# Kernel tuning notes

Hardware: AMD Instinct MI355X
Metric: run time of the kernel (lower is better)

Reference implementation:

```python
import jax, jax.numpy as jnp
import numpy as np

N_NODES = 50000
N_EDGES = 1600000
IN_FEATS = 128
H_FEATS = 128


def setup_inputs() -> dict:
    key = jax.random.key(0)
    ks = jax.random.split(key, 10)
    feat = jax.random.normal(ks[0], (N_NODES, IN_FEATS), dtype=jnp.float32)
    src = jax.random.randint(ks[1], (N_EDGES,), 0, N_NODES, dtype=jnp.int32)
    dst = jax.random.randint(ks[2], (N_EDGES,), 0, N_NODES, dtype=jnp.int32)
    s1 = 1.0 / np.sqrt(IN_FEATS)
    s2 = 1.0 / np.sqrt(H_FEATS)
    W_self1 = jax.random.uniform(ks[3], (IN_FEATS, H_FEATS), jnp.float32, -s1, s1)
    W_neigh1 = jax.random.uniform(ks[4], (IN_FEATS, H_FEATS), jnp.float32, -s1, s1)
    b1 = jnp.zeros((H_FEATS,), jnp.float32)
    W_self2 = jax.random.uniform(ks[5], (H_FEATS, H_FEATS), jnp.float32, -s2, s2)
    W_neigh2 = jax.random.uniform(ks[6], (H_FEATS, H_FEATS), jnp.float32, -s2, s2)
    b2 = jnp.zeros((H_FEATS,), jnp.float32)
    W_fc = jax.random.uniform(ks[7], (H_FEATS, IN_FEATS), jnp.float32, -s2, s2)
    b_fc = jax.random.uniform(ks[8], (IN_FEATS,), jnp.float32, -s2, s2)
    return {
        "feat": feat, "src": src, "dst": dst,
        "W_self1": W_self1, "W_neigh1": W_neigh1, "b1": b1,
        "W_self2": W_self2, "W_neigh2": W_neigh2, "b2": b2,
        "W_fc": W_fc, "b_fc": b_fc,
    }


def _mean_agg(h, src, dst):
    # segment-mean of src features onto dst nodes; zero-in-degree -> 0 (deg clamped to 1)
    msg = jnp.take(h, src, axis=0)                      # [E, d] gather (irregular)
    summ = jax.ops.segment_sum(msg, dst, num_segments=N_NODES)  # [N, d]
    deg = jax.ops.segment_sum(jnp.ones((src.shape[0],), h.dtype), dst, num_segments=N_NODES)
    return summ / jnp.maximum(deg, 1.0)[:, None]


def _sage(h, src, dst, W_self, W_neigh, b):
    h_neigh = _mean_agg(h, src, dst)
    return h @ W_self + h_neigh @ W_neigh + b


def reference(feat, src, dst, W_self1, W_neigh1, b1, W_self2, W_neigh2, b2, W_fc, b_fc):
    h = _sage(feat, src, dst, W_self1, W_neigh1, b1)
    h = jax.nn.relu(h)
    h = _sage(h, src, dst, W_self2, W_neigh2, b2)
    return h @ W_fc + b_fc
```

## Files before the change

kernel.cpp:

```cpp
#include <hip/hip_runtime.h>
#include <hip/hip_bf16.h>

#define NN 50000
#define NPAD 50008
#define NE 1600000
#define F 128
#define CAP 96
#define NBUCK 391
#define BCAP 5120
#define PADIDX 0xC350C350u

typedef short short8 __attribute__((ext_vector_type(8)));
typedef float f32x4 __attribute__((ext_vector_type(4)));
typedef float f32x2 __attribute__((ext_vector_type(2)));
typedef unsigned short u16x4 __attribute__((ext_vector_type(4)));
typedef unsigned short u16x8 __attribute__((ext_vector_type(8)));

__device__ inline unsigned short bf16rne(float f) {
  unsigned u = __builtin_bit_cast(unsigned, f);
  u += 0x7FFFu + ((u >> 16) & 1u);
  return (unsigned short)(u >> 16);
}
__device__ inline float bf16f(unsigned short s) {
  unsigned u = ((unsigned)s) << 16;
  return __builtin_bit_cast(float, u);
}
__device__ inline float bflo(unsigned v) { return __builtin_bit_cast(float, v << 16); }
__device__ inline float bfhi(unsigned v) { return __builtin_bit_cast(float, v & 0xFFFF0000u); }

__global__ void zero_misc(int* __restrict__ gcur, unsigned short* __restrict__ hbf) {
  int i = threadIdx.x;
  if (i < NBUCK) gcur[i] = 0;
  int p = i >> 7, r = NN + ((i >> 4) & 7), d = i & 15;
  ((unsigned*)hbf)[((size_t)p * NPAD + r) * 16 + d] = 0u;
}

__global__ void compose_all(const float* __restrict__ Ws2, const float* __restrict__ Wn2,
                            const float* __restrict__ b2, const float* __restrict__ Wfc,
                            const float* __restrict__ bfc,
                            float* __restrict__ wsf, float* __restrict__ wnf,
                            float* __restrict__ bfF) {
  int blk = blockIdx.x;
  int t = threadIdx.x;
  if (blk == 128) {
    if (t < 128) {
      float s = bfc[t];
      for (int k = 0; k < 128; ++k) s += b2[k] * Wfc[k * 128 + t];
      bfF[t] = s;
    }
    return;
  }
  const float* A = (blk < 64) ? Ws2 : Wn2;
  float* O = (blk < 64) ? wsf : wnf;
  int idx = (blk & 63) * 256 + t;
  int k = idx >> 7, n = idx & 127;
  float s = 0.f;
  for (int j = 0; j < 128; ++j) s += A[k * 128 + j] * Wfc[j * 128 + n];
  O[idx] = s;
}

__global__ void wprep_all(const float* __restrict__ Ws1, const float* __restrict__ Wn1,
                          const float* __restrict__ wsf, const float* __restrict__ wnf,
                          unsigned short* __restrict__ w1hi, unsigned short* __restrict__ w1lo,
                          unsigned short* __restrict__ w2hi, unsigned short* __restrict__ w2lo) {
  int blk = blockIdx.x;
  int i = (blk & 127) * 256 + threadIdx.x;
  int k = i & 255;
  int n = i >> 8;
  const float* Ws = (blk < 128) ? Ws1 : wsf;
  const float* Wn = (blk < 128) ? Wn1 : wnf;
  unsigned short* hi = (blk < 128) ? w1hi : w2hi;
  unsigned short* lo = (blk < 128) ? w1lo : w2lo;
  float w = (k < 128) ? Ws[(size_t)k * F + n] : Wn[(size_t)(k - 128) * F + n];
  unsigned short h = bf16rne(w);
  hi[i] = h;
  lo[i] = bf16rne(w - bf16f(h));
}


__global__ __launch_bounds__(256) void ebin_scatter(const int* __restrict__ src,
                                                    const int* __restrict__ dst,
                                                    int* __restrict__ gcur,
                                                    unsigned* __restrict__ ebin) {
  __shared__ int lh[512], lbase[512], lcur[512];
  int t = threadIdx.x;
  lh[t] = 0; lh[t + 256] = 0;
  lcur[t] = 0; lcur[t + 256] = 0;
  __syncthreads();
  int base = blockIdx.x * 3125;
  for (int k = t; k < 3125; k += 256) atomicAdd(&lh[dst[base + k] >> 7], 1);
  __syncthreads();
  if (t < NBUCK && lh[t]) lbase[t] = atomicAdd(&gcur[t], lh[t]);
  int t2 = t + 256;
  if (t2 < NBUCK && lh[t2]) lbase[t2] = atomicAdd(&gcur[t2], lh[t2]);
  __syncthreads();
  for (int k = t; k < 3125; k += 256) {
    int d = dst[base + k];
    int b = d >> 7;
    int off = lbase[b] + atomicAdd(&lcur[b], 1);
    if (off < BCAP)
      ebin[(size_t)b * BCAP + off] = ((unsigned)(d & 127) << 16) | (unsigned)src[base + k];
  }
}

__global__ __launch_bounds__(256) void bucket_csr(const unsigned* __restrict__ ebin,
                                                  const int* __restrict__ gcur,
                                                  int* __restrict__ cnt,
                                                  unsigned short* __restrict__ esrcPad) {
  __shared__ int lcnt[128];
  __shared__ unsigned short rows[128 * CAP];
  int t = threadIdx.x;
  int b = blockIdx.x;
  if (t < 128) lcnt[t] = 0;
  unsigned* rz = (unsigned*)rows;
  for (int i = t; i < (128 * CAP) / 2; i += 256) rz[i] = PADIDX;
  __syncthreads();
  int ecount = min(gcur[b], BCAP);
  const unsigned* eb = ebin + (size_t)b * BCAP;
  for (int i = t; i < ecount; i += 256) {
    unsigned v = eb[i];
    int dl = v >> 16;
    int p = atomicAdd(&lcnt[dl], 1);
    if (p < CAP) rows[dl * CAP + p] = (unsigned short)(v & 0xFFFFu);
  }
  __syncthreads();
  int node = b * 128 + t;
  if (t < 128 && node < NN) cnt[node] = lcnt[t];
  int nvalid = min(128, NN - b * 128);
  int limit = (nvalid * CAP) >> 1;
  unsigned* gdst = (unsigned*)(esrcPad + (size_t)b * 128 * CAP);
  for (int i = t; i < limit; i += 256) gdst[i] = rz[i];
}

__global__ void tobf16_chunk(const float* __restrict__ in,
                             unsigned short* __restrict__ chk,
                             unsigned short* __restrict__ X) {
  int i = blockIdx.x * 256 + threadIdx.x;
  if (i >= NN * 32) return;
  int node = i >> 5;
  int q = i & 31;
  int p = q >> 3;
  float4 v = ((const float4*)in)[i];
  u16x4 o;
  o[0] = bf16rne(v.x);
  o[1] = bf16rne(v.y);
  o[2] = bf16rne(v.z);
  o[3] = bf16rne(v.w);
  ((u16x4*)chk)[((size_t)p * NPAD + node) * 8 + (q & 7)] = o;
  *(u16x4*)(X + (size_t)node * 256 + q * 4) = o;
}

__global__ __launch_bounds__(256) void agg_all(const char* __restrict__ tbl,
                                               const int* __restrict__ cnt,
                                               const unsigned short* __restrict__ esrcPad,
                                               unsigned short* __restrict__ X) {
  int bid = blockIdx.x;
  int xcd = bid & 7;
  int pass = xcd & 3;
  int nodeBase = (bid >> 3) * 32 + ((xcd >> 2) & 1) * 16;
  int t = threadIdx.x;
  int node = nodeBase + (t >> 4);
  if (node >= NN) return;
  const char* tblp = tbl + (size_t)pass * NPAD * 64 + (t & 15) * 4;
  int e = cnt[node];
  if (e > CAP) e = CAP;
  const unsigned short* ep = esrcPad + (size_t)node * CAP;
  f32x2 acc0 = {0.f, 0.f}, acc1 = {0.f, 0.f};
  int nb = (e + 15) >> 4;
  for (int b = 0; b < nb; ++b) {
    u16x8 ua = *(const u16x8*)(ep + b * 16);
    u16x8 ub = *(const u16x8*)(ep + b * 16 + 8);
    unsigned v[16];
#pragma unroll
    for (int j = 0; j < 8; ++j)
      v[j] = *(const unsigned*)(tblp + (unsigned)ua[j] * 64u);
#pragma unroll
    for (int j = 0; j < 8; ++j)
      v[8 + j] = *(const unsigned*)(tblp + (unsigned)ub[j] * 64u);
#pragma unroll
    for (int j = 0; j < 16; ++j) {
      f32x2 w = {bflo(v[j]), bfhi(v[j])};
      if (j & 1) acc1 += w; else acc0 += w;
    }
  }
  f32x2 s = acc0 + acc1;
  float inv = 1.0f / (float)max(e, 1);
  unsigned w = (unsigned)bf16rne(s[0] * inv) | ((unsigned)bf16rne(s[1] * inv) << 16);
  *(unsigned*)(X + (size_t)node * 256 + 128 + pass * 32 + (t & 15) * 2) = w;
}

template <bool RELU, bool L1>
__global__ __launch_bounds__(512) void combine_mfma(
    const unsigned short* __restrict__ X,
    const unsigned short* __restrict__ WThi, const unsigned short* __restrict__ WTlo,
    const float* __restrict__ bias, float* __restrict__ Cf,
    unsigned short* __restrict__ Xout, unsigned short* __restrict__ Cb) {
  __shared__ unsigned short whs[64 * 256];
  __shared__ unsigned short wls[64 * 256];
  const int K = 256;
  int t = threadIdx.x;
  int colHalf = blockIdx.x & 1;

  {
    const unsigned short* gh = WThi + (size_t)colHalf * 64 * K;
    const unsigned short* gl = WTlo + (size_t)colHalf * 64 * K;
#pragma unroll
    for (int c = 0; c < 4; ++c) {
      int idx8 = c * 512 + t;
      int cl = idx8 >> 5;
      int byte_off = (idx8 & 31) * 16;
      int swz = byte_off ^ ((cl & 7) << 4);
      *(short8*)((char*)whs + cl * 512 + swz) = *(const short8*)(gh + (size_t)idx8 * 8);
      *(short8*)((char*)wls + cl * 512 + swz) = *(const short8*)(gl + (size_t)idx8 * 8);
    }
  }
  __syncthreads();

  int wave = t >> 6;
  int lane = t & 63;
  int lm = lane & 15;
  int lk = lane >> 4;
  int R0 = (blockIdx.x >> 1) * 128 + wave * 16;
  if (R0 < NN) {
    int rA = R0 + lm;
    if (rA >= NN) rA = NN - 1;
    short8 a[8];
    const unsigned short* xp = X + (size_t)rA * K + lk * 8;
#pragma unroll
    for (int ks = 0; ks < 8; ++ks) a[ks] = *(const short8*)(xp + ks * 32);

    f32x4 acc[4];
#pragma unroll
    for (int ct = 0; ct < 4; ++ct) {
      float b = bias[colHalf * 64 + ct * 16 + lm];
      acc[ct] = (f32x4){b, b, b, b};
    }

#pragma unroll
    for (int ct = 0; ct < 4; ++ct) {
      int cl = ct * 16 + lm;
      int cbase = cl * 512;
      int cswz = (cl & 7) << 4;
#pragma unroll
      for (int ks = 0; ks < 8; ++ks) {
        int off = cbase + ((ks * 64 + lk * 16) ^ cswz);
        short8 wh = *(const short8*)((const char*)whs + off);
        short8 wl = *(const short8*)((const char*)wls + off);
        acc[ct] = __builtin_amdgcn_mfma_f32_16x16x32_bf16(a[ks], wh, acc[ct], 0, 0, 0);
        acc[ct] = __builtin_amdgcn_mfma_f32_16x16x32_bf16(a[ks], wl, acc[ct], 0, 0, 0);
      }
    }

#pragma unroll
    for (int ct = 0; ct < 4; ++ct) {
#pragma unroll
      for (int r = 0; r < 4; ++r) {
        int row = R0 + lk * 4 + r;
        if (row < NN) {
          float v = acc[ct][r];
          if (RELU) v = fmaxf(v, 0.f);
          int col = colHalf * 64 + ct * 16 + lm;
          if (L1) {
            unsigned short b = bf16rne(v);
            Xout[(size_t)row * 256 + col] = b;
            Cb[((size_t)(col >> 5) * NPAD + row) * 32 + (col & 31)] = b;
          } else {
            Cf[(size_t)row * F + col] = v;
          }
        }
      }
    }
  }
}

extern "C" void kernel_launch(void* const* d_in, const int* in_sizes, int n_in,
                              void* d_out, int out_size, void* d_ws, size_t ws_size,
                              hipStream_t stream) {
  const float* feat = (const float*)d_in[0];
  const int* src = (const int*)d_in[1];
  const int* dst = (const int*)d_in[2];
  const float* Ws1 = (const float*)d_in[3];
  const float* Wn1 = (const float*)d_in[4];
  const float* b1 = (const float*)d_in[5];
  const float* Ws2 = (const float*)d_in[6];
  const float* Wn2 = (const float*)d_in[7];
  const float* b2 = (const float*)d_in[8];
  const float* Wfc = (const float*)d_in[9];
  const float* bfc = (const float*)d_in[10];
  float* out = (float*)d_out;

  unsigned short* esrcPad = (unsigned short*)d_ws;
  int* cnt = (int*)(esrcPad + (size_t)NN * CAP);
  int* gcur = cnt + 50048;
  unsigned short* X1 = (unsigned short*)(gcur + 512);
  unsigned short* X2 = X1 + (size_t)NN * 256;
  unsigned* ebin = (unsigned*)X2;
  unsigned short* w1hi = X2 + (size_t)NN * 256;
  unsigned short* w1lo = w1hi + 128 * 256;
  unsigned short* w2hi = w1lo + 128 * 256;
  unsigned short* w2lo = w2hi + 128 * 256;
  float* wsf = (float*)(w2lo + 128 * 256);
  float* wnf = wsf + 128 * 128;
  float* bfF = wnf + 128 * 128;
  unsigned short* hbf = (unsigned short*)(bfF + 128);

  compose_all<<<129, 256, 0, stream>>>(Ws2, Wn2, b2, Wfc, bfc, wsf, wnf, bfF);
  wprep_all<<<256, 256, 0, stream>>>(Ws1, Wn1, wsf, wnf, w1hi, w1lo, w2hi, w2lo);
  zero_misc<<<1, 512, 0, stream>>>(gcur, hbf);
  tobf16_chunk<<<(NN * 32 + 255) / 256, 256, 0, stream>>>(feat, hbf, X1);

  ebin_scatter<<<512, 256, 0, stream>>>(src, dst, gcur, ebin);
  bucket_csr<<<NBUCK, 256, 0, stream>>>(ebin, gcur, cnt, esrcPad);

  const int aggBlocks = 1563 * 8;
  const int gemBlocks = ((NN + 127) / 128) * 2;

  agg_all<<<aggBlocks, 256, 0, stream>>>((const char*)hbf, cnt, esrcPad, X1);
  combine_mfma<true, true><<<gemBlocks, 512, 0, stream>>>(X1, w1hi, w1lo, b1,
                                                          nullptr, X2, hbf);

  agg_all<<<aggBlocks, 256, 0, stream>>>((const char*)hbf, cnt, esrcPad, X2);
  combine_mfma<false, false><<<gemBlocks, 512, 0, stream>>>(X2, w2hi, w2lo, bfF,
                                                            out, nullptr, nullptr);
}
```

Before: 173.9 us.

## Sort nodes by degree bucket for aggregation and fuse weight composition into prep

Adds a two-kernel counting sort that orders nodes by their 16-edge batch count, and the aggregation kernel walks nodes through this permutation so lanes in a wavefront process nodes with similar degree. This targets divergence and load imbalance in the gather loop. It also folds the Ws2/Wn2·Wfc composition into the weight-prep kernel, removing one launch and intermediate buffers. In exchange it adds two small launches, an indirect index load, and less locality in output row writes.

Result: slower. 184.8 us (+6.3%).

```diff
diff --git a/kernel.cpp b/kernel.cpp
--- a/kernel.cpp
+++ b/kernel.cpp
@@ -30,19 +30,21 @@
 
 __global__ void zero_misc(int* __restrict__ gcur, unsigned short* __restrict__ hbf) {
   int i = threadIdx.x;
-  if (i < NBUCK) gcur[i] = 0;
+  gcur[i] = 0;
   int p = i >> 7, r = NN + ((i >> 4) & 7), d = i & 15;
   ((unsigned*)hbf)[((size_t)p * NPAD + r) * 16 + d] = 0u;
 }
 
-__global__ void compose_all(const float* __restrict__ Ws2, const float* __restrict__ Wn2,
-                            const float* __restrict__ b2, const float* __restrict__ Wfc,
-                            const float* __restrict__ bfc,
-                            float* __restrict__ wsf, float* __restrict__ wnf,
-                            float* __restrict__ bfF) {
+__global__ void wprep_all(const float* __restrict__ Ws1, const float* __restrict__ Wn1,
+                          const float* __restrict__ Ws2, const float* __restrict__ Wn2,
+                          const float* __restrict__ b2, const float* __restrict__ Wfc,
+                          const float* __restrict__ bfc,
+                          unsigned short* __restrict__ w1hi, unsigned short* __restrict__ w1lo,
+                          unsigned short* __restrict__ w2hi, unsigned short* __restrict__ w2lo,
+                          float* __restrict__ bfF) {
   int blk = blockIdx.x;
   int t = threadIdx.x;
-  if (blk == 128) {
+  if (blk == 256) {
     if (t < 128) {
       float s = bfc[t];
       for (int k = 0; k < 128; ++k) s += b2[k] * Wfc[k * 128 + t];
@@ -50,29 +52,22 @@
     }
     return;
   }
-  const float* A = (blk < 64) ? Ws2 : Wn2;
-  float* O = (blk < 64) ? wsf : wnf;
-  int idx = (blk & 63) * 256 + t;
-  int k = idx >> 7, n = idx & 127;
-  float s = 0.f;
-  for (int j = 0; j < 128; ++j) s += A[k * 128 + j] * Wfc[j * 128 + n];
-  O[idx] = s;
-}
-
-__global__ void wprep_all(const float* __restrict__ Ws1, const float* __restrict__ Wn1,
-                          const float* __restrict__ wsf, const float* __restrict__ wnf,
-                          unsigned short* __restrict__ w1hi, unsigned short* __restrict__ w1lo,
-                          unsigned short* __restrict__ w2hi, unsigned short* __restrict__ w2lo) {
-  int blk = blockIdx.x;
-  int i = (blk & 127) * 256 + threadIdx.x;
+  int i = (blk & 127) * 256 + t;
   int k = i & 255;
   int n = i >> 8;
-  const float* Ws = (blk < 128) ? Ws1 : wsf;
-  const float* Wn = (blk < 128) ? Wn1 : wnf;
+  float w;
+  if (blk < 128) {
+    w = (k < 128) ? Ws1[(size_t)k * F + n] : Wn1[(size_t)(k - 128) * F + n];
+  } else {
+    const float* A = (k < 128) ? Ws2 : Wn2;
+    int kk = k & 127;
+    float s = 0.f;
+    for (int j = 0; j < 128; ++j) s += A[kk * 128 + j] * Wfc[j * 128 + n];
+    w = s;
+  }
+  unsigned short h = bf16rne(w);
   unsigned short* hi = (blk < 128) ? w1hi : w2hi;
   unsigned short* lo = (blk < 128) ? w1lo : w2lo;
-  float w = (k < 128) ? Ws[(size_t)k * F + n] : Wn[(size_t)(k - 128) * F + n];
-  unsigned short h = bf16rne(w);
   hi[i] = h;
   lo[i] = bf16rne(w - bf16f(h));
 }
@@ -130,6 +125,43 @@
   int limit = (nvalid * CAP) >> 1;
   unsigned* gdst = (unsigned*)(esrcPad + (size_t)b * 128 * CAP);
   for (int i = t; i < limit; i += 256) gdst[i] = rz[i];
+}
+
+
+__global__ void deg_hist(const int* __restrict__ cnt, int* __restrict__ gbin) {
+  __shared__ int lh[8];
+  int t = threadIdx.x;
+  if (t < 8) lh[t] = 0;
+  __syncthreads();
+  int node = blockIdx.x * 256 + t;
+  if (node < NN) atomicAdd(&lh[(min(cnt[node], CAP) + 15) >> 4], 1);
+  __syncthreads();
+  if (t < 8 && lh[t]) atomicAdd(&gbin[t], lh[t]);
+}
+
+__global__ void deg_scatter(const int* __restrict__ cnt, const int* __restrict__ gbin,
+                            int* __restrict__ gcur2, int* __restrict__ order) {
+  __shared__ int lh[8], lbase[8], lcur[8];
+  int t = threadIdx.x;
+  if (t < 8) { lh[t] = 0; lcur[t] = 0; }
+  __syncthreads();
+  int node = blockIdx.x * 256 + t;
+  int nb = 0;
+  if (node < NN) {
+    nb = (min(cnt[node], CAP) + 15) >> 4;
+    atomicAdd(&lh[nb], 1);
+  }
+  __syncthreads();
+  if (t < 8) {
+    int base = 0;
+    for (int j = 0; j < t; ++j) base += gbin[j];
+    lbase[t] = lh[t] ? base + atomicAdd(&gcur2[t], lh[t]) : 0;
+  }
+  __syncthreads();
+  if (node < NN) {
+    int off = atomicAdd(&lcur[nb], 1);
+    order[lbase[nb] + off] = node;
+  }
 }
 
 __global__ void tobf16_chunk(const float* __restrict__ in,
@@ -153,14 +185,16 @@
 __global__ __launch_bounds__(256) void agg_all(const char* __restrict__ tbl,
                                                const int* __restrict__ cnt,
                                                const unsigned short* __restrict__ esrcPad,
+                                               const int* __restrict__ order,
                                                unsigned short* __restrict__ X) {
   int bid = blockIdx.x;
   int xcd = bid & 7;
   int pass = xcd & 3;
   int nodeBase = (bid >> 3) * 32 + ((xcd >> 2) & 1) * 16;
   int t = threadIdx.x;
-  int node = nodeBase + (t >> 4);
-  if (node >= NN) return;
+  int idx = nodeBase + (t >> 4);
+  if (idx >= NN) return;
+  int node = order[idx];
   const char* tblp = tbl + (size_t)pass * NPAD * 64 + (t & 15) * 4;
   int e = cnt[node];
   if (e > CAP) e = CAP;
@@ -292,34 +326,37 @@
   unsigned short* esrcPad = (unsigned short*)d_ws;
   int* cnt = (int*)(esrcPad + (size_t)NN * CAP);
   int* gcur = cnt + 50048;
-  unsigned short* X1 = (unsigned short*)(gcur + 512);
+  int* gbin = gcur + 400;
+  int* gcur2 = gcur + 408;
+  int* order = gcur + 512;
+  unsigned short* X1 = (unsigned short*)(order + NN);
   unsigned short* X2 = X1 + (size_t)NN * 256;
   unsigned* ebin = (unsigned*)X2;
   unsigned short* w1hi = X2 + (size_t)NN * 256;
   unsigned short* w1lo = w1hi + 128 * 256;
   unsigned short* w2hi = w1lo + 128 * 256;
   unsigned short* w2lo = w2hi + 128 * 256;
-  float* wsf = (float*)(w2lo + 128 * 256);
-  float* wnf = wsf + 128 * 128;
-  float* bfF = wnf + 128 * 128;
+  float* bfF = (float*)(w2lo + 128 * 256);
   unsigned short* hbf = (unsigned short*)(bfF + 128);
 
-  compose_all<<<129, 256, 0, stream>>>(Ws2, Wn2, b2, Wfc, bfc, wsf, wnf, bfF);
-  wprep_all<<<256, 256, 0, stream>>>(Ws1, Wn1, wsf, wnf, w1hi, w1lo, w2hi, w2lo);
+  wprep_all<<<257, 256, 0, stream>>>(Ws1, Wn1, Ws2, Wn2, b2, Wfc, bfc,
+                                     w1hi, w1lo, w2hi, w2lo, bfF);
   zero_misc<<<1, 512, 0, stream>>>(gcur, hbf);
   tobf16_chunk<<<(NN * 32 + 255) / 256, 256, 0, stream>>>(feat, hbf, X1);
 
   ebin_scatter<<<512, 256, 0, stream>>>(src, dst, gcur, ebin);
   bucket_csr<<<NBUCK, 256, 0, stream>>>(ebin, gcur, cnt, esrcPad);
+  deg_hist<<<196, 256, 0, stream>>>(cnt, gbin);
+  deg_scatter<<<196, 256, 0, stream>>>(cnt, gbin, gcur2, order);
 
   const int aggBlocks = 1563 * 8;
   const int gemBlocks = ((NN + 127) / 128) * 2;
 
-  agg_all<<<aggBlocks, 256, 0, stream>>>((const char*)hbf, cnt, esrcPad, X1);
+  agg_all<<<aggBlocks, 256, 0, stream>>>((const char*)hbf, cnt, esrcPad, order, X1);
   combine_mfma<true, true><<<gemBlocks, 512, 0, stream>>>(X1, w1hi, w1lo, b1,
                                                           nullptr, X2, hbf);
 
-  agg_all<<<aggBlocks, 256, 0, stream>>>((const char*)hbf, cnt, esrcPad, X2);
+  agg_all<<<aggBlocks, 256, 0, stream>>>((const char*)hbf, cnt, esrcPad, order, X2);
   combine_mfma<false, false><<<gemBlocks, 512, 0, stream>>>(X2, w2hi, w2lo, bfF,
                                                             out, nullptr, nullptr);
 }
```
